# Performance work log

Measured on AMD Instinct MI355X. Metric: run time of the kernel, lower is better.

## Reference

```python
import jax, jax.numpy as jnp
import numpy as np

D_MODEL, NUM_HEADS, ROPE_DIM = 256, 8, 16
B_GRAPHS, N_MAX = 16, 512


def _make_batch():
    # ragged graph sizes between 256 and 512 atoms; contiguous, sorted ids
    sizes = np.array([256 + (i * 256) // 15 for i in range(B_GRAPHS)], dtype=np.int64)
    return np.repeat(np.arange(B_GRAPHS), sizes)  # total N = 6137


def setup_inputs() -> dict:
    key = jax.random.key(0)
    ks = jax.random.split(key, 6)
    batch_np = _make_batch()
    N = int(batch_np.shape[0])
    x = jax.random.normal(ks[0], (N, D_MODEL), jnp.float32)
    pos = jax.random.normal(ks[1], (N, 3), jnp.float32) * 3.0
    W_qkv = jax.random.normal(ks[2], (D_MODEL, 3 * D_MODEL), jnp.float32) / np.sqrt(D_MODEL).astype(np.float32)
    W_out = jax.random.normal(ks[3], (D_MODEL, D_MODEL), jnp.float32) / np.sqrt(D_MODEL).astype(np.float32)
    rope_freqs = jax.random.normal(ks[4], (ROPE_DIM,), jnp.float32) * 0.1
    W_rope = jax.random.normal(ks[5], (ROPE_DIM, NUM_HEADS), jnp.float32) / np.sqrt(ROPE_DIM).astype(np.float32)
    gamma = jnp.ones((D_MODEL,), jnp.float32)
    beta = jnp.zeros((D_MODEL,), jnp.float32)
    return {"x": x, "pos": pos, "batch": jnp.asarray(batch_np, jnp.int32),
            "W_qkv": W_qkv, "W_out": W_out, "rope_freqs": rope_freqs,
            "W_rope": W_rope, "gamma": gamma, "beta": beta,
            "B": B_GRAPHS, "n_max": N_MAX}


def _forward(x, pos, W_qkv, W_out, rope_freqs, W_rope, gamma, beta, batch, B, n_max):
    N, d = x.shape
    H = W_rope.shape[1]
    hd = d // H
    scale = hd ** -0.5
    # pad ragged graphs to [B, n_max] via vectorized scatter (batch is sorted)
    sizes = jax.ops.segment_sum(jnp.ones((N,), jnp.int32), batch, num_segments=B)
    offsets = jnp.concatenate([jnp.zeros((1,), jnp.int32), jnp.cumsum(sizes)[:-1].astype(jnp.int32)])
    pidx = jnp.arange(N, dtype=jnp.int32) - offsets[batch]  # position within graph
    x_pad = jnp.zeros((B, n_max, d), x.dtype).at[batch, pidx].set(x)
    pos_pad = jnp.zeros((B, n_max, 3), pos.dtype).at[batch, pidx].set(pos)
    pad = jnp.ones((B, n_max), bool).at[batch, pidx].set(False)  # True = padding
    # multi-head self-attention on scalar channel
    qkv = x_pad @ W_qkv  # [B, n, 3d]
    q, k, v = jnp.split(qkv, 3, axis=-1)
    heads = lambda t: t.reshape(B, n_max, H, hd).transpose(0, 2, 1, 3)  # [B,H,n,hd]
    q, k, v = heads(q), heads(k), heads(v)
    logits = jnp.einsum('bhid,bhjd->bhij', q, k) * scale
    # Euclidean RoPE distance bias: rope_proj(cos(|omega| * ||r_i - r_j||))
    diff = pos_pad[:, :, None, :] - pos_pad[:, None, :, :]  # [B,n,n,3]
    sq = jnp.sum(diff * diff, axis=-1)
    dist = jnp.where(sq > 0, jnp.sqrt(jnp.where(sq > 0, sq, 1.0)), 0.0)  # safe norm
    fourier = jnp.cos(dist[..., None] * jnp.abs(rope_freqs))  # [B,n,n,r]
    bias = jnp.einsum('bijr,rh->bhij', fourier, W_rope)
    pair_pad = (pad[:, :, None] | pad[:, None, :])[:, None]  # [B,1,n,n]
    bias = jnp.where(pair_pad, 0.0, bias)
    logits = jnp.where(pad[:, None, None, :], -1e9, logits + bias)
    attn = jax.nn.softmax(logits, axis=-1)
    out = jnp.einsum('bhij,bhjd->bhid', attn, v)
    out = out.transpose(0, 2, 1, 3).reshape(B, n_max, d) @ W_out
    out_flat = out[batch, pidx]  # gather back to flat node list
    # residual + LayerNorm (eps = 1e-5)
    y = x + out_flat
    mu = jnp.mean(y, axis=-1, keepdims=True)
    var = jnp.mean((y - mu) ** 2, axis=-1, keepdims=True)
    return gamma * (y - mu) * jax.lax.rsqrt(var + 1e-5) + beta


def reference(x, pos, batch, W_qkv, W_out, rope_freqs, W_rope, gamma, beta, B, n_max):
    return _forward(x, pos, W_qkv, W_out, rope_freqs, W_rope, gamma, beta, batch, B, n_max)
```

## Files before the change

### kernel.cpp

```cpp
#include <hip/hip_runtime.h>
#include <hip/hip_bf16.h>

typedef __hip_bfloat16 bf16;
typedef short bf16x8 __attribute__((ext_vector_type(8)));
typedef float f32x4 __attribute__((ext_vector_type(4)));

#define NGRAPH 16
#define QSCALE 0.17677669529663687f
#define VT_LD 8192

struct __align__(16) bf8x { bf16 v[8]; };

__global__ __launch_bounds__(256) void k_prep(const float* __restrict__ x,
                                              const float* __restrict__ Wqkv,
                                              const float* __restrict__ Wout,
                                              const int* __restrict__ batch,
                                              bf16* __restrict__ xb,
                                              bf16* __restrict__ Wqkv_t,
                                              bf16* __restrict__ Wout_t,
                                              int* __restrict__ offs, int N) {
  int tid = blockIdx.x * 256 + threadIdx.x;
  int T = gridDim.x * 256;
  for (int i = tid; i < N * 256; i += T) xb[i] = __float2bfloat16(x[i]);
  for (int i = tid; i < 768 * 256; i += T) {
    int n = i >> 8, k = i & 255;
    Wqkv_t[i] = __float2bfloat16(Wqkv[k * 768 + n]);
  }
  for (int i = tid; i < 256 * 256; i += T) {
    int n = i >> 8, k = i & 255;
    Wout_t[i] = __float2bfloat16(Wout[k * 256 + n]);
  }
  for (int i = tid; i < N; i += T) {
    if (i == 0) { offs[0] = 0; offs[NGRAPH] = N; }
    else if (batch[i] != batch[i - 1]) offs[batch[i]] = i;
  }
}

__global__ __launch_bounds__(256) void k_bias(const float* __restrict__ pos,
                                              const float* __restrict__ freqs,
                                              const float* __restrict__ Wrope,
                                              const int* __restrict__ offs,
                                              bf16* __restrict__ bias) {
  __shared__ float Sb[8][16][33];
  __shared__ float wf[16];
  __shared__ float Wr[16][8];
  int b = blockIdx.z;
  int off = offs[b], n = offs[b + 1] - off;
  int q0 = blockIdx.x * 16, j0 = blockIdx.y * 32;
  if (q0 >= n || j0 >= n) return;
  int t = threadIdx.x;
  if (t < 16) wf[t] = fabsf(freqs[t]);
  if (t < 128) Wr[t >> 3][t & 7] = Wrope[t];
  int tb = 0;
  for (int g = 0; g < b; ++g) {
    int ng = offs[g + 1] - offs[g];
    tb += ((ng + 15) >> 4) * ((ng + 31) >> 5);
  }
  int jtiles = (n + 31) >> 5;
  bf16* tile = bias + (size_t)(tb + (q0 >> 4) * jtiles + (j0 >> 5)) * 4096;
  int qs = t >> 5, j = t & 31;
  int jg = j0 + j; bool vj = jg < n;
  float jx, jy, jz;
  { int a = (vj ? off + jg : off) * 3; jx = pos[a]; jy = pos[a + 1]; jz = pos[a + 2]; }
  __syncthreads();
  #pragma unroll
  for (int e = 0; e < 2; ++e) {
    int q = qs + 8 * e; int qg = q0 + q; bool vq = qg < n;
    float bv[8];
    #pragma unroll
    for (int h = 0; h < 8; ++h) bv[h] = 0.f;
    if (vq && vj) {
      int a = (off + qg) * 3;
      float dx = pos[a] - jx, dy = pos[a + 1] - jy, dz = pos[a + 2] - jz;
      float dist = sqrtf(dx * dx + dy * dy + dz * dz);
      #pragma unroll
      for (int r = 0; r < 16; ++r) {
        float cv = __cosf(dist * wf[r]);
        #pragma unroll
        for (int h = 0; h < 8; ++h) bv[h] += cv * Wr[r][h];
      }
    }
    #pragma unroll
    for (int h = 0; h < 8; ++h) Sb[h][q][j] = (vq && vj) ? bv[h] : -1e30f;
  }
  __syncthreads();
  int w = t >> 6, l = t & 63, fq = l >> 4, fr = l & 15;
  #pragma unroll
  for (int hh = 0; hh < 2; ++hh) {
    int h = w * 2 + hh;
    __align__(16) bf16 pk[8];
    #pragma unroll
    for (int k = 0; k < 8; ++k)
      pk[k] = __float2bfloat16(Sb[h][fq * 4 + (k & 3)][(k >> 2) * 16 + fr]);
    *(bf16x8*)(tile + h * 512 + l * 8) = *(const bf16x8*)pk;
  }
}

__global__ __launch_bounds__(256) void k_gemm_qkv(const bf16* __restrict__ A,
                                                  const bf16* __restrict__ Bt,
                                                  const int* __restrict__ batch,
                                                  const int* __restrict__ offs,
                                                  bf16* __restrict__ C,
                                                  bf16* __restrict__ VT, int M) {
  __shared__ float tr[64][65];
  __shared__ int rowcol[64];
  int t = threadIdx.x, w = t >> 6, l = t & 63, fr = l & 15, fq = l >> 4;
  int m0 = blockIdx.x * 64, n0 = blockIdx.y * 64;
  bool isV = (n0 >= 512);
  if (isV && t < 64) {
    int m = m0 + t; if (m > M - 1) m = M - 1;
    int b = batch[m];
    rowcol[t] = b * 512 + (m - offs[b]);
  }
  int arow = m0 + w * 16 + fr; if (arow > M - 1) arow = M - 1;
  bf16x8 af[8];
  #pragma unroll
  for (int kt = 0; kt < 8; ++kt)
    af[kt] = *(const bf16x8*)(A + (size_t)arow * 256 + kt * 32 + fq * 8);
  f32x4 acc[4];
  #pragma unroll
  for (int nt = 0; nt < 4; ++nt) acc[nt] = (f32x4){0.f, 0.f, 0.f, 0.f};
  #pragma unroll
  for (int nt = 0; nt < 4; ++nt) {
    int brow = n0 + nt * 16 + fr;
    #pragma unroll
    for (int kt = 0; kt < 8; ++kt) {
      bf16x8 bf_ = *(const bf16x8*)(Bt + (size_t)brow * 256 + kt * 32 + fq * 8);
      acc[nt] = __builtin_amdgcn_mfma_f32_16x16x32_bf16(af[kt], bf_, acc[nt], 0, 0, 0);
    }
  }
  #pragma unroll
  for (int nt = 0; nt < 4; ++nt) {
    int col = n0 + nt * 16 + fr;
    float sc = (col < 256) ? QSCALE : 1.f;
    #pragma unroll
    for (int rr = 0; rr < 4; ++rr) {
      int m = m0 + w * 16 + fq * 4 + rr;
      if (m < M) C[(size_t)m * 768 + col] = __float2bfloat16(acc[nt][rr] * sc);
    }
  }
  if (isV) {
    #pragma unroll
    for (int nt = 0; nt < 4; ++nt)
      #pragma unroll
      for (int rr = 0; rr < 4; ++rr)
        tr[nt * 16 + fr][w * 16 + fq * 4 + rr] = acc[nt][rr];
    __syncthreads();
    int c = t >> 2, r0 = (t & 3) * 16;
    int dg = (n0 - 512) + c;
    #pragma unroll
    for (int i = 0; i < 16; ++i) {
      int r = r0 + i;
      VT[(size_t)dg * VT_LD + rowcol[r]] = __float2bfloat16(tr[c][r]);
    }
  }
}

__global__ __launch_bounds__(256) void k_attn(const bf16* __restrict__ QKVb,
                                              const bf16* __restrict__ VT,
                                              const bf16* __restrict__ bias,
                                              const int* __restrict__ offs,
                                              bf16* __restrict__ Ob) {
  __shared__ __align__(16) bf16 Pt[4][16][40];
  int b = blockIdx.y, hbase = blockIdx.z * 4;
  int off = offs[b], n = offs[b + 1] - off;
  int q0 = blockIdx.x * 16;
  if (q0 >= n) return;
  int t = threadIdx.x, w = t >> 6, l = t & 63, fr = l & 15, fq = l >> 4;
  int h = hbase + w;
  int tb = 0;
  for (int g = 0; g < b; ++g) {
    int ng = offs[g + 1] - offs[g];
    tb += ((ng + 15) >> 4) * ((ng + 31) >> 5);
  }
  int jtiles = (n + 31) >> 5;
  const bf16* btile = bias + (size_t)(tb + (q0 >> 4) * jtiles) * 4096 + h * 512 + l * 8;
  const bf16* Kb = QKVb + (size_t)off * 768 + 256 + h * 32 + fq * 8;
  const bf16* Vb = VT + (size_t)(h * 32 + fr) * VT_LD + b * 512 + fq * 8;
  int qrow = q0 + fr; bool qv = qrow < n;
  bf16x8 aq = *(const bf16x8*)(QKVb + (size_t)(qv ? off + qrow : off) * 768 + h * 32 + fq * 8);
  if (!qv) aq = (bf16x8){0, 0, 0, 0, 0, 0, 0, 0};
  f32x4 Oa[2];
  Oa[0] = (f32x4){0.f, 0.f, 0.f, 0.f}; Oa[1] = (f32x4){0.f, 0.f, 0.f, 0.f};
  float lacc[4] = {0.f, 0.f, 0.f, 0.f};

#define LOADT(JT, B_, K0_, K1_, V0_, V1_) do {                                   \
    int _jt = (JT); int _k0 = _jt * 32 + fr, _k1 = _k0 + 16;                     \
    B_ = *(const bf8x*)(btile + (size_t)_jt * 4096);                             \
    K0_ = *(const bf16x8*)(Kb + (size_t)((_k0 < n) ? _k0 : 0) * 768);            \
    K1_ = *(const bf16x8*)(Kb + (size_t)((_k1 < n) ? _k1 : 0) * 768);            \
    V0_ = *(const bf16x8*)(Vb + _jt * 32);                                       \
    V1_ = *(const bf16x8*)(Vb + (size_t)16 * VT_LD + _jt * 32);                  \
  } while (0)

  bf8x cb; bf16x8 ck0, ck1, cv0, cv1;
  LOADT(0, cb, ck0, ck1, cv0, cv1);
  for (int jt = 0; jt < jtiles; ++jt) {
    bf8x nb; bf16x8 nk0, nk1, nv0, nv1;
    if (jt + 1 < jtiles) LOADT(jt + 1, nb, nk0, nk1, nv0, nv1);
    f32x4 z = {0.f, 0.f, 0.f, 0.f};
    f32x4 S0 = __builtin_amdgcn_mfma_f32_16x16x32_bf16(aq, ck0, z, 0, 0, 0);
    f32x4 S1 = __builtin_amdgcn_mfma_f32_16x16x32_bf16(aq, ck1, z, 0, 0, 0);
    #pragma unroll
    for (int k = 0; k < 8; ++k) {
      int jti = k >> 2, rr = k & 3;
      float s = (jti ? S1[rr] : S0[rr]) + __bfloat162float(cb.v[k]);
      float p = __expf(s);
      lacc[rr] += p;
      Pt[w][fq * 4 + rr][jti * 16 + fr] = __float2bfloat16(p);
    }
    bf16x8 ap = *(const bf16x8*)&Pt[w][fr][fq * 8];
    Oa[0] = __builtin_amdgcn_mfma_f32_16x16x32_bf16(ap, cv0, Oa[0], 0, 0, 0);
    Oa[1] = __builtin_amdgcn_mfma_f32_16x16x32_bf16(ap, cv1, Oa[1], 0, 0, 0);
    cb = nb; ck0 = nk0; ck1 = nk1; cv0 = nv0; cv1 = nv1;
  }
#undef LOADT
  #pragma unroll
  for (int rr = 0; rr < 4; ++rr) {
    #pragma unroll
    for (int m2 = 1; m2 <= 8; m2 <<= 1) lacc[rr] += __shfl_xor(lacc[rr], m2);
  }
  #pragma unroll
  for (int dh = 0; dh < 2; ++dh)
    #pragma unroll
    for (int rr = 0; rr < 4; ++rr) {
      int row = q0 + fq * 4 + rr;
      if (row < n)
        Ob[(size_t)(off + row) * 256 + h * 32 + dh * 16 + fr] =
            __float2bfloat16(Oa[dh][rr] / lacc[rr]);
    }
}

__global__ __launch_bounds__(256) void k_attn_fb(const float* __restrict__ pos,
                                                 const float* __restrict__ freqs,
                                                 const float* __restrict__ Wrope,
                                                 const bf16* __restrict__ QKVb,
                                                 const bf16* __restrict__ VT,
                                                 const int* __restrict__ offs,
                                                 bf16* __restrict__ Ob) {
  __shared__ float Sb[2][4][16][34];
  __shared__ __align__(16) bf16 Pt[4][16][40];
  __shared__ float wf[16];
  __shared__ float Wr[16][4];
  int b = blockIdx.y, hbase = blockIdx.z * 4;
  int off = offs[b], n = offs[b + 1] - off;
  int q0 = blockIdx.x * 16;
  if (q0 >= n) return;
  int t = threadIdx.x, w = t >> 6, l = t & 63, fr = l & 15, fq = l >> 4;
  int h = hbase + w;
  if (t < 16) wf[t] = fabsf(freqs[t]);
  if (t < 64) Wr[t >> 2][t & 3] = Wrope[(t >> 2) * 8 + hbase + (t & 3)];
  int qrow = q0 + fr; bool qv = qrow < n;
  bf16x8 aq = *(const bf16x8*)(QKVb + (size_t)((qv ? off + qrow : off)) * 768 + h * 32 + fq * 8);
  if (!qv) aq = (bf16x8){0, 0, 0, 0, 0, 0, 0, 0};
  int bq = t >> 5, bj = t & 31;
  float qpx[2], qpy[2], qpz[2]; bool bqv[2];
  #pragma unroll
  for (int e = 0; e < 2; ++e) {
    int qq = q0 + bq + 8 * e; bqv[e] = qq < n;
    int a = (bqv[e] ? off + qq : off) * 3;
    qpx[e] = pos[a]; qpy[e] = pos[a + 1]; qpz[e] = pos[a + 2];
  }
  float m_st[4], l_st[4]; f32x4 Oa[2];
  #pragma unroll
  for (int rr = 0; rr < 4; ++rr) { m_st[rr] = -1e30f; l_st[rr] = 0.f; }
  Oa[0] = (f32x4){0.f, 0.f, 0.f, 0.f}; Oa[1] = (f32x4){0.f, 0.f, 0.f, 0.f};
  __syncthreads();
  int par = 0;
  for (int j0 = 0; j0 < n; j0 += 32, par ^= 1) {
    {
      int jg = j0 + bj; bool vj = jg < n;
      int a = (vj ? off + jg : off) * 3;
      float jx = pos[a], jy = pos[a + 1], jz = pos[a + 2];
      #pragma unroll
      for (int e = 0; e < 2; ++e) {
        float bv0 = 0.f, bv1 = 0.f, bv2 = 0.f, bv3 = 0.f;
        if (vj && bqv[e]) {
          float dx = qpx[e] - jx, dy = qpy[e] - jy, dz = qpz[e] - jz;
          float dist = sqrtf(dx * dx + dy * dy + dz * dz);
          #pragma unroll
          for (int r = 0; r < 16; ++r) {
            float cv = __cosf(dist * wf[r]);
            bv0 += cv * Wr[r][0]; bv1 += cv * Wr[r][1];
            bv2 += cv * Wr[r][2]; bv3 += cv * Wr[r][3];
          }
        }
        int qi = bq + 8 * e;
        Sb[par][0][qi][bj] = vj ? bv0 : -1e30f;
        Sb[par][1][qi][bj] = vj ? bv1 : -1e30f;
        Sb[par][2][qi][bj] = vj ? bv2 : -1e30f;
        Sb[par][3][qi][bj] = vj ? bv3 : -1e30f;
      }
    }
    __syncthreads();
    f32x4 Sv[2];
    #pragma unroll
    for (int jt = 0; jt < 2; ++jt) {
      int krow = j0 + jt * 16 + fr;
      bf16x8 bk = *(const bf16x8*)(QKVb + (size_t)((krow < n) ? off + krow : off) * 768 + 256 + h * 32 + fq * 8);
      f32x4 z = {0.f, 0.f, 0.f, 0.f};
      Sv[jt] = __builtin_amdgcn_mfma_f32_16x16x32_bf16(aq, bk, z, 0, 0, 0);
      #pragma unroll
      for (int rr = 0; rr < 4; ++rr) Sv[jt][rr] += Sb[par][w][fq * 4 + rr][jt * 16 + fr];
    }
    #pragma unroll
    for (int rr = 0; rr < 4; ++rr) {
      float mrow = fmaxf(Sv[0][rr], Sv[1][rr]);
      #pragma unroll
      for (int m2 = 1; m2 <= 8; m2 <<= 1) mrow = fmaxf(mrow, __shfl_xor(mrow, m2));
      float mnew = fmaxf(m_st[rr], mrow);
      float al = __expf(m_st[rr] - mnew);
      m_st[rr] = mnew;
      float p0 = __expf(Sv[0][rr] - mnew), p1 = __expf(Sv[1][rr] - mnew);
      Sv[0][rr] = p0; Sv[1][rr] = p1;
      float rs = p0 + p1;
      #pragma unroll
      for (int m2 = 1; m2 <= 8; m2 <<= 1) rs += __shfl_xor(rs, m2);
      l_st[rr] = l_st[rr] * al + rs;
      Oa[0][rr] *= al; Oa[1][rr] *= al;
    }
    #pragma unroll
    for (int jt = 0; jt < 2; ++jt)
      #pragma unroll
      for (int rr = 0; rr < 4; ++rr)
        Pt[w][fq * 4 + rr][jt * 16 + fr] = __float2bfloat16(Sv[jt][rr]);
    bf16x8 ap = *(const bf16x8*)&Pt[w][fr][fq * 8];
    #pragma unroll
    for (int dh = 0; dh < 2; ++dh) {
      bf16x8 bv = *(const bf16x8*)(VT + (size_t)(h * 32 + dh * 16 + fr) * VT_LD + b * 512 + j0 + fq * 8);
      Oa[dh] = __builtin_amdgcn_mfma_f32_16x16x32_bf16(ap, bv, Oa[dh], 0, 0, 0);
    }
  }
  #pragma unroll
  for (int dh = 0; dh < 2; ++dh)
    #pragma unroll
    for (int rr = 0; rr < 4; ++rr) {
      int row = q0 + fq * 4 + rr;
      if (row < n)
        Ob[(size_t)(off + row) * 256 + h * 32 + dh * 16 + fr] =
            __float2bfloat16(Oa[dh][rr] / l_st[rr]);
    }
}

__global__ __launch_bounds__(256) void k_gemm_out_ln(const bf16* __restrict__ A,
                                                     const bf16* __restrict__ Bt,
                                                     const float* __restrict__ x,
                                                     const float* __restrict__ gamma,
                                                     const float* __restrict__ beta,
                                                     float* __restrict__ out, int M) {
  int t = threadIdx.x, w = t >> 6, l = t & 63, fr = l & 15, fq = l >> 4;
  int m0 = blockIdx.x * 64;
  int arow = m0 + w * 16 + fr; if (arow > M - 1) arow = M - 1;
  bf16x8 af[8];
  #pragma unroll
  for (int kt = 0; kt < 8; ++kt)
    af[kt] = *(const bf16x8*)(A + (size_t)arow * 256 + kt * 32 + fq * 8);
  f32x4 acc[16];
  #pragma unroll
  for (int nt = 0; nt < 16; ++nt) {
    acc[nt] = (f32x4){0.f, 0.f, 0.f, 0.f};
    int brow = nt * 16 + fr;
    #pragma unroll
    for (int kt = 0; kt < 8; ++kt) {
      bf16x8 bf_ = *(const bf16x8*)(Bt + (size_t)brow * 256 + kt * 32 + fq * 8);
      acc[nt] = __builtin_amdgcn_mfma_f32_16x16x32_bf16(af[kt], bf_, acc[nt], 0, 0, 0);
    }
  }
  float g[16], bb[16];
  #pragma unroll
  for (int nt = 0; nt < 16; ++nt) { g[nt] = gamma[nt * 16 + fr]; bb[nt] = beta[nt * 16 + fr]; }
  #pragma unroll
  for (int rr = 0; rr < 4; ++rr) {
    int row = m0 + w * 16 + fq * 4 + rr;
    int rc = (row < M) ? row : (M - 1);
    float vv[16];
    float s = 0.f, ss = 0.f;
    #pragma unroll
    for (int nt = 0; nt < 16; ++nt) {
      float y = acc[nt][rr] + x[(size_t)rc * 256 + nt * 16 + fr];
      vv[nt] = y; s += y; ss += y * y;
    }
    #pragma unroll
    for (int m2 = 1; m2 <= 8; m2 <<= 1) { s += __shfl_xor(s, m2); ss += __shfl_xor(ss, m2); }
    float mean = s * (1.f / 256.f);
    float var = ss * (1.f / 256.f) - mean * mean;
    float rstd = rsqrtf(var + 1e-5f);
    if (row < M) {
      #pragma unroll
      for (int nt = 0; nt < 16; ++nt)
        out[(size_t)row * 256 + nt * 16 + fr] = g[nt] * (vv[nt] - mean) * rstd + bb[nt];
    }
  }
}

extern "C" void kernel_launch(void* const* d_in, const int* in_sizes, int n_in,
                              void* d_out, int out_size, void* d_ws, size_t ws_size,
                              hipStream_t stream) {
  (void)n_in; (void)out_size;
  const float* x     = (const float*)d_in[0];
  const float* pos   = (const float*)d_in[1];
  const int*   batch = (const int*)d_in[2];
  const float* Wqkv  = (const float*)d_in[3];
  const float* Wout  = (const float*)d_in[4];
  const float* freqs = (const float*)d_in[5];
  const float* Wrope = (const float*)d_in[6];
  const float* gamma = (const float*)d_in[7];
  const float* beta  = (const float*)d_in[8];
  float* out = (float*)d_out;

  int N = in_sizes[0] / 256;

  char* base = (char*)d_ws;
  int*   offs   = (int*)base;
  bf16*  QKVb   = (bf16*)(base + 1024);
  bf16*  VT     = (bf16*)(base + 9427456);
  bf16*  xb     = (bf16*)(base + 13621760);
  bf16*  Wqkv_t = (bf16*)(base + 16763904);
  bf16*  Wout_t = (bf16*)(base + 17157120);
  bf16*  biasb  = (bf16*)(base + 17288192);
  bf16*  Ob     = xb;

  bool fast = ws_size >= (size_t)58700000;

  int MB = (N + 63) / 64;
  k_prep<<<1024, 256, 0, stream>>>(x, Wqkv, Wout, batch, xb, Wqkv_t, Wout_t, offs, N);
  if (fast)
    k_bias<<<dim3(32, 16, NGRAPH), 256, 0, stream>>>(pos, freqs, Wrope, offs, biasb);
  k_gemm_qkv<<<dim3(MB, 12), 256, 0, stream>>>(xb, Wqkv_t, batch, offs, QKVb, VT, N);
  if (fast)
    k_attn<<<dim3(32, NGRAPH, 2), 256, 0, stream>>>(QKVb, VT, biasb, offs, Ob);
  else
    k_attn_fb<<<dim3(32, NGRAPH, 2), 256, 0, stream>>>(pos, freqs, Wrope, QKVb, VT, offs, Ob);
  k_gemm_out_ln<<<MB, 256, 0, stream>>>(Ob, Wout_t, x, gamma, beta, out, N);
}
```

Before: 205.4 us.

## Merge bias and QKV GEMM into one launch, fuse x cast, split out-proj LN

```diff
diff --git a/kernel.cpp b/kernel.cpp
--- a/kernel.cpp
+++ b/kernel.cpp
@@ -11,147 +11,170 @@
 
 struct __align__(16) bf8x { bf16 v[8]; };
 
-__global__ __launch_bounds__(256) void k_prep(const float* __restrict__ x,
-                                              const float* __restrict__ Wqkv,
-                                              const float* __restrict__ Wout,
-                                              const int* __restrict__ batch,
-                                              bf16* __restrict__ xb,
-                                              bf16* __restrict__ Wqkv_t,
-                                              bf16* __restrict__ Wout_t,
-                                              int* __restrict__ offs, int N) {
-  int tid = blockIdx.x * 256 + threadIdx.x;
-  int T = gridDim.x * 256;
-  for (int i = tid; i < N * 256; i += T) xb[i] = __float2bfloat16(x[i]);
-  for (int i = tid; i < 768 * 256; i += T) {
-    int n = i >> 8, k = i & 255;
-    Wqkv_t[i] = __float2bfloat16(Wqkv[k * 768 + n]);
-  }
-  for (int i = tid; i < 256 * 256; i += T) {
-    int n = i >> 8, k = i & 255;
-    Wout_t[i] = __float2bfloat16(Wout[k * 256 + n]);
-  }
-  for (int i = tid; i < N; i += T) {
-    if (i == 0) { offs[0] = 0; offs[NGRAPH] = N; }
-    else if (batch[i] != batch[i - 1]) offs[batch[i]] = i;
-  }
-}
-
-__global__ __launch_bounds__(256) void k_bias(const float* __restrict__ pos,
-                                              const float* __restrict__ freqs,
-                                              const float* __restrict__ Wrope,
-                                              const int* __restrict__ offs,
-                                              bf16* __restrict__ bias) {
-  __shared__ float Sb[8][16][33];
+__device__ __forceinline__ bf16x8 ldcvt8(const float* p) {
+  float4 u = *(const float4*)p, v = *(const float4*)(p + 4);
+  __align__(16) bf16 tmp[8];
+  tmp[0] = __float2bfloat16(u.x); tmp[1] = __float2bfloat16(u.y);
+  tmp[2] = __float2bfloat16(u.z); tmp[3] = __float2bfloat16(u.w);
+  tmp[4] = __float2bfloat16(v.x); tmp[5] = __float2bfloat16(v.y);
+  tmp[6] = __float2bfloat16(v.z); tmp[7] = __float2bfloat16(v.w);
+  return *(const bf16x8*)tmp;
+}
+
+__global__ __launch_bounds__(256) void k_pre(const float* __restrict__ Wqkv,
+                                             const float* __restrict__ Wout,
+                                             const int* __restrict__ batch,
+                                             bf16* __restrict__ Wqkv_t,
+                                             bf16* __restrict__ Wout_t,
+                                             int* __restrict__ offs, int N) {
+  __shared__ float ld[64][65];
+  int bid = blockIdx.x, t = threadIdx.x;
+  int c = t & 63, r0 = t >> 6;
+  if (bid < 48) {
+    int k0 = (bid & 3) * 64, n0 = (bid >> 2) * 64;
+    #pragma unroll
+    for (int r = r0; r < 64; r += 4) ld[r][c] = Wqkv[(size_t)(k0 + r) * 768 + n0 + c];
+    __syncthreads();
+    #pragma unroll
+    for (int r = r0; r < 64; r += 4)
+      Wqkv_t[(size_t)(n0 + r) * 256 + k0 + c] = __float2bfloat16(ld[c][r]);
+  } else if (bid < 64) {
+    int b2 = bid - 48;
+    int k0 = (b2 & 3) * 64, n0 = (b2 >> 2) * 64;
+    #pragma unroll
+    for (int r = r0; r < 64; r += 4) ld[r][c] = Wout[(size_t)(k0 + r) * 256 + n0 + c];
+    __syncthreads();
+    #pragma unroll
+    for (int r = r0; r < 64; r += 4)
+      Wout_t[(size_t)(n0 + r) * 256 + k0 + c] = __float2bfloat16(ld[c][r]);
+  } else {
+    for (int i = t; i < N; i += 256) {
+      if (i == 0) { offs[0] = 0; offs[NGRAPH] = N; }
+      else if (batch[i] != batch[i - 1]) offs[batch[i]] = i;
+    }
+  }
+}
+
+__global__ __launch_bounds__(256) void k_mid(const float* __restrict__ x,
+                                             const bf16* __restrict__ Wqkv_t,
+                                             const float* __restrict__ pos,
+                                             const float* __restrict__ freqs,
+                                             const float* __restrict__ Wrope,
+                                             const int* __restrict__ batch,
+                                             const int* __restrict__ offs,
+                                             bf16* __restrict__ QKVb,
+                                             bf16* __restrict__ VT,
+                                             bf16* __restrict__ bias,
+                                             int N, int MBm) {
+  __shared__ __align__(16) char smem[16896];
   __shared__ float wf[16];
   __shared__ float Wr[16][8];
-  int b = blockIdx.z;
-  int off = offs[b], n = offs[b + 1] - off;
-  int q0 = blockIdx.x * 16, j0 = blockIdx.y * 32;
-  if (q0 >= n || j0 >= n) return;
-  int t = threadIdx.x;
-  if (t < 16) wf[t] = fabsf(freqs[t]);
-  if (t < 128) Wr[t >> 3][t & 7] = Wrope[t];
-  int tb = 0;
-  for (int g = 0; g < b; ++g) {
-    int ng = offs[g + 1] - offs[g];
-    tb += ((ng + 15) >> 4) * ((ng + 31) >> 5);
-  }
-  int jtiles = (n + 31) >> 5;
-  bf16* tile = bias + (size_t)(tb + (q0 >> 4) * jtiles + (j0 >> 5)) * 4096;
-  int qs = t >> 5, j = t & 31;
-  int jg = j0 + j; bool vj = jg < n;
-  float jx, jy, jz;
-  { int a = (vj ? off + jg : off) * 3; jx = pos[a]; jy = pos[a + 1]; jz = pos[a + 2]; }
-  __syncthreads();
-  #pragma unroll
-  for (int e = 0; e < 2; ++e) {
-    int q = qs + 8 * e; int qg = q0 + q; bool vq = qg < n;
-    float bv[8];
-    #pragma unroll
-    for (int h = 0; h < 8; ++h) bv[h] = 0.f;
-    if (vq && vj) {
-      int a = (off + qg) * 3;
-      float dx = pos[a] - jx, dy = pos[a + 1] - jy, dz = pos[a + 2] - jz;
-      float dist = sqrtf(dx * dx + dy * dy + dz * dz);
-      #pragma unroll
-      for (int r = 0; r < 16; ++r) {
-        float cv = __cosf(dist * wf[r]);
+  int t = threadIdx.x, bid = blockIdx.x;
+  int nbg = MBm * 12;
+  if (bid < nbg) {
+    float (*tr)[65] = (float(*)[65])smem;
+    int* rowcol = (int*)(smem + 16640);
+    int w = t >> 6, l = t & 63, fr = l & 15, fq = l >> 4;
+    int m0 = (bid % MBm) * 64, n0 = (bid / MBm) * 64;
+    bool isV = (n0 >= 512);
+    if (isV && t < 64) {
+      int m = m0 + t; if (m > N - 1) m = N - 1;
+      int b = batch[m];
+      rowcol[t] = b * 512 + (m - offs[b]);
+    }
+    int arow = m0 + w * 16 + fr; if (arow > N - 1) arow = N - 1;
+    bf16x8 af[8];
+    #pragma unroll
+    for (int kt = 0; kt < 8; ++kt)
+      af[kt] = ldcvt8(x + (size_t)arow * 256 + kt * 32 + fq * 8);
+    f32x4 acc[4];
+    #pragma unroll
+    for (int nt = 0; nt < 4; ++nt) acc[nt] = (f32x4){0.f, 0.f, 0.f, 0.f};
+    #pragma unroll
+    for (int nt = 0; nt < 4; ++nt) {
+      int brow = n0 + nt * 16 + fr;
+      #pragma unroll
+      for (int kt = 0; kt < 8; ++kt) {
+        bf16x8 bf_ = *(const bf16x8*)(Wqkv_t + (size_t)brow * 256 + kt * 32 + fq * 8);
+        acc[nt] = __builtin_amdgcn_mfma_f32_16x16x32_bf16(af[kt], bf_, acc[nt], 0, 0, 0);
+      }
+    }
+    #pragma unroll
+    for (int nt = 0; nt < 4; ++nt) {
+      int col = n0 + nt * 16 + fr;
+      float sc = (col < 256) ? QSCALE : 1.f;
+      #pragma unroll
+      for (int rr = 0; rr < 4; ++rr) {
+        int m = m0 + w * 16 + fq * 4 + rr;
+        if (m < N) QKVb[(size_t)m * 768 + col] = __float2bfloat16(acc[nt][rr] * sc);
+      }
+    }
+    if (isV) {
+      #pragma unroll
+      for (int nt = 0; nt < 4; ++nt)
         #pragma unroll
-        for (int h = 0; h < 8; ++h) bv[h] += cv * Wr[r][h];
-      }
-    }
-    #pragma unroll
-    for (int h = 0; h < 8; ++h) Sb[h][q][j] = (vq && vj) ? bv[h] : -1e30f;
-  }
-  __syncthreads();
-  int w = t >> 6, l = t & 63, fq = l >> 4, fr = l & 15;
-  #pragma unroll
-  for (int hh = 0; hh < 2; ++hh) {
-    int h = w * 2 + hh;
-    __align__(16) bf16 pk[8];
-    #pragma unroll
-    for (int k = 0; k < 8; ++k)
-      pk[k] = __float2bfloat16(Sb[h][fq * 4 + (k & 3)][(k >> 2) * 16 + fr]);
-    *(bf16x8*)(tile + h * 512 + l * 8) = *(const bf16x8*)pk;
-  }
-}
-
-__global__ __launch_bounds__(256) void k_gemm_qkv(const bf16* __restrict__ A,
-                                                  const bf16* __restrict__ Bt,
-                                                  const int* __restrict__ batch,
-                                                  const int* __restrict__ offs,
-                                                  bf16* __restrict__ C,
-                                                  bf16* __restrict__ VT, int M) {
-  __shared__ float tr[64][65];
-  __shared__ int rowcol[64];
-  int t = threadIdx.x, w = t >> 6, l = t & 63, fr = l & 15, fq = l >> 4;
-  int m0 = blockIdx.x * 64, n0 = blockIdx.y * 64;
-  bool isV = (n0 >= 512);
-  if (isV && t < 64) {
-    int m = m0 + t; if (m > M - 1) m = M - 1;
-    int b = batch[m];
-    rowcol[t] = b * 512 + (m - offs[b]);
-  }
-  int arow = m0 + w * 16 + fr; if (arow > M - 1) arow = M - 1;
-  bf16x8 af[8];
-  #pragma unroll
-  for (int kt = 0; kt < 8; ++kt)
-    af[kt] = *(const bf16x8*)(A + (size_t)arow * 256 + kt * 32 + fq * 8);
-  f32x4 acc[4];
-  #pragma unroll
-  for (int nt = 0; nt < 4; ++nt) acc[nt] = (f32x4){0.f, 0.f, 0.f, 0.f};
-  #pragma unroll
-  for (int nt = 0; nt < 4; ++nt) {
-    int brow = n0 + nt * 16 + fr;
-    #pragma unroll
-    for (int kt = 0; kt < 8; ++kt) {
-      bf16x8 bf_ = *(const bf16x8*)(Bt + (size_t)brow * 256 + kt * 32 + fq * 8);
-      acc[nt] = __builtin_amdgcn_mfma_f32_16x16x32_bf16(af[kt], bf_, acc[nt], 0, 0, 0);
-    }
-  }
-  #pragma unroll
-  for (int nt = 0; nt < 4; ++nt) {
-    int col = n0 + nt * 16 + fr;
-    float sc = (col < 256) ? QSCALE : 1.f;
-    #pragma unroll
-    for (int rr = 0; rr < 4; ++rr) {
-      int m = m0 + w * 16 + fq * 4 + rr;
-      if (m < M) C[(size_t)m * 768 + col] = __float2bfloat16(acc[nt][rr] * sc);
-    }
-  }
-  if (isV) {
-    #pragma unroll
-    for (int nt = 0; nt < 4; ++nt)
-      #pragma unroll
-      for (int rr = 0; rr < 4; ++rr)
-        tr[nt * 16 + fr][w * 16 + fq * 4 + rr] = acc[nt][rr];
+        for (int rr = 0; rr < 4; ++rr)
+          tr[nt * 16 + fr][w * 16 + fq * 4 + rr] = acc[nt][rr];
+      __syncthreads();
+      int c = t >> 2, r0 = (t & 3) * 16;
+      int dg = (n0 - 512) + c;
+      #pragma unroll
+      for (int i = 0; i < 16; ++i) {
+        int r = r0 + i;
+        VT[(size_t)dg * VT_LD + rowcol[r]] = __float2bfloat16(tr[c][r]);
+      }
+    }
+  } else {
+    float (*Sb)[16][33] = (float(*)[16][33])smem;
+    int b2 = bid - nbg;
+    int b = b2 >> 9;
+    int q0 = (b2 & 31) * 16, j0 = ((b2 >> 5) & 15) * 32;
+    int off = offs[b], n = offs[b + 1] - off;
+    if (q0 >= n || j0 >= n) return;
+    if (t < 16) wf[t] = fabsf(freqs[t]);
+    if (t < 128) Wr[t >> 3][t & 7] = Wrope[t];
+    int tb = 0;
+    for (int g = 0; g < b; ++g) {
+      int ng = offs[g + 1] - offs[g];
+      tb += ((ng + 15) >> 4) * ((ng + 31) >> 5);
+    }
+    int jtiles = (n + 31) >> 5;
+    bf16* tile = bias + (size_t)(tb + (q0 >> 4) * jtiles + (j0 >> 5)) * 4096;
+    int qs = t >> 5, j = t & 31;
+    int jg = j0 + j; bool vj = jg < n;
+    float jx, jy, jz;
+    { int a = (vj ? off + jg : off) * 3; jx = pos[a]; jy = pos[a + 1]; jz = pos[a + 2]; }
     __syncthreads();
-    int c = t >> 2, r0 = (t & 3) * 16;
-    int dg = (n0 - 512) + c;
-    #pragma unroll
-    for (int i = 0; i < 16; ++i) {
-      int r = r0 + i;
-      VT[(size_t)dg * VT_LD + rowcol[r]] = __float2bfloat16(tr[c][r]);
+    #pragma unroll
+    for (int e = 0; e < 2; ++e) {
+      int q = qs + 8 * e; int qg = q0 + q; bool vq = qg < n;
+      float bv[8];
+      #pragma unroll
+      for (int h = 0; h < 8; ++h) bv[h] = 0.f;
+      if (vq && vj) {
+        int a = (off + qg) * 3;
+        float dx = pos[a] - jx, dy = pos[a + 1] - jy, dz = pos[a + 2] - jz;
+        float dist = sqrtf(dx * dx + dy * dy + dz * dz);
+        #pragma unroll
+        for (int r = 0; r < 16; ++r) {
+          float cv = __cosf(dist * wf[r]);
+          #pragma unroll
+          for (int h = 0; h < 8; ++h) bv[h] += cv * Wr[r][h];
+        }
+      }
+      #pragma unroll
+      for (int h = 0; h < 8; ++h) Sb[h][q][j] = (vq && vj) ? bv[h] : -1e30f;
+    }
+    __syncthreads();
+    int w = t >> 6, l = t & 63, fq = l >> 4, fr = l & 15;
+    #pragma unroll
+    for (int hh = 0; hh < 2; ++hh) {
+      int h = w * 2 + hh;
+      __align__(16) bf16 pk[8];
+      #pragma unroll
+      for (int k = 0; k < 8; ++k)
+        pk[k] = __float2bfloat16(Sb[h][fq * 4 + (k & 3)][(k >> 2) * 16 + fr]);
+      *(bf16x8*)(tile + h * 512 + l * 8) = *(const bf16x8*)pk;
     }
   }
 }
@@ -231,164 +254,62 @@
     }
 }
 
-__global__ __launch_bounds__(256) void k_attn_fb(const float* __restrict__ pos,
-                                                 const float* __restrict__ freqs,
-                                                 const float* __restrict__ Wrope,
-                                                 const bf16* __restrict__ QKVb,
-                                                 const bf16* __restrict__ VT,
-                                                 const int* __restrict__ offs,
-                                                 bf16* __restrict__ Ob) {
-  __shared__ float Sb[2][4][16][34];
-  __shared__ __align__(16) bf16 Pt[4][16][40];
-  __shared__ float wf[16];
-  __shared__ float Wr[16][4];
-  int b = blockIdx.y, hbase = blockIdx.z * 4;
-  int off = offs[b], n = offs[b + 1] - off;
-  int q0 = blockIdx.x * 16;
-  if (q0 >= n) return;
+__global__ __launch_bounds__(256) void k_out_ln(const bf16* __restrict__ A,
+                                                const bf16* __restrict__ Bt,
+                                                const float* __restrict__ x,
+                                                const float* __restrict__ gamma,
+                                                const float* __restrict__ beta,
+                                                float* __restrict__ out, int M) {
+  __shared__ float ps[4][16], pss[4][16];
   int t = threadIdx.x, w = t >> 6, l = t & 63, fr = l & 15, fq = l >> 4;
-  int h = hbase + w;
-  if (t < 16) wf[t] = fabsf(freqs[t]);
-  if (t < 64) Wr[t >> 2][t & 3] = Wrope[(t >> 2) * 8 + hbase + (t & 3)];
-  int qrow = q0 + fr; bool qv = qrow < n;
-  bf16x8 aq = *(const bf16x8*)(QKVb + (size_t)((qv ? off + qrow : off)) * 768 + h * 32 + fq * 8);
-  if (!qv) aq = (bf16x8){0, 0, 0, 0, 0, 0, 0, 0};
-  int bq = t >> 5, bj = t & 31;
-  float qpx[2], qpy[2], qpz[2]; bool bqv[2];
-  #pragma unroll
-  for (int e = 0; e < 2; ++e) {
-    int qq = q0 + bq + 8 * e; bqv[e] = qq < n;
-    int a = (bqv[e] ? off + qq : off) * 3;
-    qpx[e] = pos[a]; qpy[e] = pos[a + 1]; qpz[e] = pos[a + 2];
-  }
-  float m_st[4], l_st[4]; f32x4 Oa[2];
-  #pragma unroll
-  for (int rr = 0; rr < 4; ++rr) { m_st[rr] = -1e30f; l_st[rr] = 0.f; }
-  Oa[0] = (f32x4){0.f, 0.f, 0.f, 0.f}; Oa[1] = (f32x4){0.f, 0.f, 0.f, 0.f};
-  __syncthreads();
-  int par = 0;
-  for (int j0 = 0; j0 < n; j0 += 32, par ^= 1) {
-    {
-      int jg = j0 + bj; bool vj = jg < n;
-      int a = (vj ? off + jg : off) * 3;
-      float jx = pos[a], jy = pos[a + 1], jz = pos[a + 2];
-      #pragma unroll
-      for (int e = 0; e < 2; ++e) {
-        float bv0 = 0.f, bv1 = 0.f, bv2 = 0.f, bv3 = 0.f;
-        if (vj && bqv[e]) {
-          float dx = qpx[e] - jx, dy = qpy[e] - jy, dz = qpz[e] - jz;
-          float dist = sqrtf(dx * dx + dy * dy + dz * dz);
-          #pragma unroll
-          for (int r = 0; r < 16; ++r) {
-            float cv = __cosf(dist * wf[r]);
-            bv0 += cv * Wr[r][0]; bv1 += cv * Wr[r][1];
-            bv2 += cv * Wr[r][2]; bv3 += cv * Wr[r][3];
-          }
-        }
-        int qi = bq + 8 * e;
-        Sb[par][0][qi][bj] = vj ? bv0 : -1e30f;
-        Sb[par][1][qi][bj] = vj ? bv1 : -1e30f;
-        Sb[par][2][qi][bj] = vj ? bv2 : -1e30f;
-        Sb[par][3][qi][bj] = vj ? bv3 : -1e30f;
-      }
-    }
-    __syncthreads();
-    f32x4 Sv[2];
-    #pragma unroll
-    for (int jt = 0; jt < 2; ++jt) {
-      int krow = j0 + jt * 16 + fr;
-      bf16x8 bk = *(const bf16x8*)(QKVb + (size_t)((krow < n) ? off + krow : off) * 768 + 256 + h * 32 + fq * 8);
-      f32x4 z = {0.f, 0.f, 0.f, 0.f};
-      Sv[jt] = __builtin_amdgcn_mfma_f32_16x16x32_bf16(aq, bk, z, 0, 0, 0);
-      #pragma unroll
-      for (int rr = 0; rr < 4; ++rr) Sv[jt][rr] += Sb[par][w][fq * 4 + rr][jt * 16 + fr];
-    }
-    #pragma unroll
-    for (int rr = 0; rr < 4; ++rr) {
-      float mrow = fmaxf(Sv[0][rr], Sv[1][rr]);
-      #pragma unroll
-      for (int m2 = 1; m2 <= 8; m2 <<= 1) mrow = fmaxf(mrow, __shfl_xor(mrow, m2));
-      float mnew = fmaxf(m_st[rr], mrow);
-      float al = __expf(m_st[rr] - mnew);
-      m_st[rr] = mnew;
-      float p0 = __expf(Sv[0][rr] - mnew), p1 = __expf(Sv[1][rr] - mnew);
-      Sv[0][rr] = p0; Sv[1][rr] = p1;
-      float rs = p0 + p1;
-      #pragma unroll
-      for (int m2 = 1; m2 <= 8; m2 <<= 1) rs += __shfl_xor(rs, m2);
-      l_st[rr] = l_st[rr] * al + rs;
-      Oa[0][rr] *= al; Oa[1][rr] *= al;
-    }
-    #pragma unroll
-    for (int jt = 0; jt < 2; ++jt)
-      #pragma unroll
-      for (int rr = 0; rr < 4; ++rr)
-        Pt[w][fq * 4 + rr][jt * 16 + fr] = __float2bfloat16(Sv[jt][rr]);
-    bf16x8 ap = *(const bf16x8*)&Pt[w][fr][fq * 8];
-    #pragma unroll
-    for (int dh = 0; dh < 2; ++dh) {
-      bf16x8 bv = *(const bf16x8*)(VT + (size_t)(h * 32 + dh * 16 + fr) * VT_LD + b * 512 + j0 + fq * 8);
-      Oa[dh] = __builtin_amdgcn_mfma_f32_16x16x32_bf16(ap, bv, Oa[dh], 0, 0, 0);
-    }
-  }
-  #pragma unroll
-  for (int dh = 0; dh < 2; ++dh)
-    #pragma unroll
-    for (int rr = 0; rr < 4; ++rr) {
-      int row = q0 + fq * 4 + rr;
-      if (row < n)
-        Ob[(size_t)(off + row) * 256 + h * 32 + dh * 16 + fr] =
-            __float2bfloat16(Oa[dh][rr] / l_st[rr]);
-    }
-}
-
-__global__ __launch_bounds__(256) void k_gemm_out_ln(const bf16* __restrict__ A,
-                                                     const bf16* __restrict__ Bt,
-                                                     const float* __restrict__ x,
-                                                     const float* __restrict__ gamma,
-                                                     const float* __restrict__ beta,
-                                                     float* __restrict__ out, int M) {
-  int t = threadIdx.x, w = t >> 6, l = t & 63, fr = l & 15, fq = l >> 4;
-  int m0 = blockIdx.x * 64;
-  int arow = m0 + w * 16 + fr; if (arow > M - 1) arow = M - 1;
+  int m0 = blockIdx.x * 16;
+  int arow = m0 + fr; if (arow > M - 1) arow = M - 1;
   bf16x8 af[8];
   #pragma unroll
   for (int kt = 0; kt < 8; ++kt)
     af[kt] = *(const bf16x8*)(A + (size_t)arow * 256 + kt * 32 + fq * 8);
-  f32x4 acc[16];
-  #pragma unroll
-  for (int nt = 0; nt < 16; ++nt) {
+  f32x4 acc[4];
+  #pragma unroll
+  for (int nt = 0; nt < 4; ++nt) {
     acc[nt] = (f32x4){0.f, 0.f, 0.f, 0.f};
-    int brow = nt * 16 + fr;
+    int brow = w * 64 + nt * 16 + fr;
     #pragma unroll
     for (int kt = 0; kt < 8; ++kt) {
       bf16x8 bf_ = *(const bf16x8*)(Bt + (size_t)brow * 256 + kt * 32 + fq * 8);
       acc[nt] = __builtin_amdgcn_mfma_f32_16x16x32_bf16(af[kt], bf_, acc[nt], 0, 0, 0);
     }
   }
-  float g[16], bb[16];
-  #pragma unroll
-  for (int nt = 0; nt < 16; ++nt) { g[nt] = gamma[nt * 16 + fr]; bb[nt] = beta[nt * 16 + fr]; }
+  float y[4][4];
   #pragma unroll
   for (int rr = 0; rr < 4; ++rr) {
-    int row = m0 + w * 16 + fq * 4 + rr;
+    int row = m0 + fq * 4 + rr;
     int rc = (row < M) ? row : (M - 1);
-    float vv[16];
     float s = 0.f, ss = 0.f;
     #pragma unroll
-    for (int nt = 0; nt < 16; ++nt) {
-      float y = acc[nt][rr] + x[(size_t)rc * 256 + nt * 16 + fr];
-      vv[nt] = y; s += y; ss += y * y;
+    for (int nt = 0; nt < 4; ++nt) {
+      float v = acc[nt][rr] + x[(size_t)rc * 256 + w * 64 + nt * 16 + fr];
+      y[rr][nt] = v; s += v; ss += v * v;
     }
     #pragma unroll
     for (int m2 = 1; m2 <= 8; m2 <<= 1) { s += __shfl_xor(s, m2); ss += __shfl_xor(ss, m2); }
+    if (fr == 0) { ps[w][fq * 4 + rr] = s; pss[w][fq * 4 + rr] = ss; }
+  }
+  __syncthreads();
+  #pragma unroll
+  for (int rr = 0; rr < 4; ++rr) {
+    int row = m0 + fq * 4 + rr;
+    int ri = fq * 4 + rr;
+    float s = ps[0][ri] + ps[1][ri] + ps[2][ri] + ps[3][ri];
+    float ss = pss[0][ri] + pss[1][ri] + pss[2][ri] + pss[3][ri];
     float mean = s * (1.f / 256.f);
     float var = ss * (1.f / 256.f) - mean * mean;
     float rstd = rsqrtf(var + 1e-5f);
     if (row < M) {
       #pragma unroll
-      for (int nt = 0; nt < 16; ++nt)
-        out[(size_t)row * 256 + nt * 16 + fr] = g[nt] * (vv[nt] - mean) * rstd + bb[nt];
+      for (int nt = 0; nt < 4; ++nt) {
+        int col = w * 64 + nt * 16 + fr;
+        out[(size_t)row * 256 + col] = gamma[col] * (y[rr][nt] - mean) * rstd + beta[col];
+      }
     }
   }
 }
@@ -396,7 +317,7 @@
 extern "C" void kernel_launch(void* const* d_in, const int* in_sizes, int n_in,
                               void* d_out, int out_size, void* d_ws, size_t ws_size,
                               hipStream_t stream) {
-  (void)n_in; (void)out_size;
+  (void)n_in; (void)out_size; (void)ws_size;
   const float* x     = (const float*)d_in[0];
   const float* pos   = (const float*)d_in[1];
   const int*   batch = (const int*)d_in[2];
@@ -414,22 +335,15 @@
   int*   offs   = (int*)base;
   bf16*  QKVb   = (bf16*)(base + 1024);
   bf16*  VT     = (bf16*)(base + 9427456);
-  bf16*  xb     = (bf16*)(base + 13621760);
-  bf16*  Wqkv_t = (bf16*)(base + 16763904);
-  bf16*  Wout_t = (bf16*)(base + 17157120);
+  bf16*  Wqkv_t = (bf16*)(base + 13621760);
+  bf16*  Wout_t = (bf16*)(base + 14014976);
+  bf16*  Ob     = (bf16*)(base + 14146048);
   bf16*  biasb  = (bf16*)(base + 17288192);
-  bf16*  Ob     = xb;
-
-  bool fast = ws_size >= (size_t)58700000;
-
-  int MB = (N + 63) / 64;
-  k_prep<<<1024, 256, 0, stream>>>(x, Wqkv, Wout, batch, xb, Wqkv_t, Wout_t, offs, N);
-  if (fast)
-    k_bias<<<dim3(32, 16, NGRAPH), 256, 0, stream>>>(pos, freqs, Wrope, offs, biasb);
-  k_gemm_qkv<<<dim3(MB, 12), 256, 0, stream>>>(xb, Wqkv_t, batch, offs, QKVb, VT, N);
-  if (fast)
-    k_attn<<<dim3(32, NGRAPH, 2), 256, 0, stream>>>(QKVb, VT, biasb, offs, Ob);
-  else
-    k_attn_fb<<<dim3(32, NGRAPH, 2), 256, 0, stream>>>(pos, freqs, Wrope, QKVb, VT, offs, Ob);
-  k_gemm_out_ln<<<MB, 256, 0, stream>>>(Ob, Wout_t, x, gamma, beta, out, N);
-}
+
+  int MBm = (N + 63) / 64;
+  k_pre<<<65, 256, 0, stream>>>(Wqkv, Wout, batch, Wqkv_t, Wout_t, offs, N);
+  k_mid<<<MBm * 12 + 8192, 256, 0, stream>>>(x, Wqkv_t, pos, freqs, Wrope, batch, offs,
+                                             QKVb, VT, biasb, N, MBm);
+  k_attn<<<dim3(32, NGRAPH, 2), 256, 0, stream>>>(QKVb, VT, biasb, offs, Ob);
+  k_out_ln<<<(N + 15) / 16, 256, 0, stream>>>(Ob, Wout_t, x, gamma, beta, out, N);
+}
```

New measurement: 189.3 us. -7.9%, faster.
